# Kernel tuning notes

Measured on AMD Instinct MI355X. Metric: run time of the kernel, lower is better.

Reference implementation:

```python
import jax, jax.numpy as jnp
import numpy as np

N, E = 100000, 1600000
C_IN, C_HID, C_OUT = 64, 128, 64
EPS_MSG = 1e-7   # GENConv message eps
EPS_BN = 1e-5    # BatchNorm eps


def setup_inputs() -> dict:
    key = jax.random.key(0)
    ks = jax.random.split(key, 8)
    glorot = lambda k, shp, fan: jax.random.normal(k, shp, jnp.float32) * (1.0 / np.sqrt(fan))
    return dict(
        x=jax.random.normal(ks[0], (N, C_IN), jnp.float32),
        edge_index=jax.random.randint(ks[1], (2, E), 0, N, jnp.int32),
        edge_attr=jax.random.normal(ks[2], (E, C_IN), jnp.float32),
        pos=jax.random.normal(ks[3], (N, 3), jnp.float32),
        # GENConv internal MLP: Linear -> BN -> ReLU -> Linear
        W1=glorot(ks[4], (C_IN, C_HID), C_IN), b1=jnp.zeros((C_HID,), jnp.float32),
        g_mlp=jnp.ones((C_HID,), jnp.float32), be_mlp=jnp.zeros((C_HID,), jnp.float32),
        W2=glorot(ks[5], (C_HID, C_OUT), C_HID), b2=jnp.zeros((C_OUT,), jnp.float32),
        # block: BN -> SiLU -> Linear(no bias) -> BN -> SiLU
        g1=jnp.ones((C_OUT,), jnp.float32), be1=jnp.zeros((C_OUT,), jnp.float32),
        Wl=glorot(ks[6], (C_OUT, C_OUT), C_OUT),
        g2=jnp.ones((C_OUT,), jnp.float32), be2=jnp.zeros((C_OUT,), jnp.float32),
    )


def _bn(h, g, b):
    # training-mode batch norm over the node dimension
    m = h.mean(0)
    v = jnp.mean((h - m) ** 2, axis=0)
    return (h - m) * jax.lax.rsqrt(v + EPS_BN) * g + b


def reference(x, edge_index, edge_attr, pos, W1, b1, g_mlp, be_mlp, W2, b2,
              g1, be1, Wl, g2, be2):
    src, dst = edge_index[0], edge_index[1]
    # GENConv message: relu(x_j + e_attr) + eps, shape [E, C_IN]
    msg = jax.nn.relu(x[src] + edge_attr) + EPS_MSG
    # softmax aggregation over incoming edges per destination node (t = 1)
    mx = jax.ops.segment_max(msg, dst, num_segments=N)
    mx = jnp.where(jnp.isfinite(mx), mx, 0.0)  # guard empty segments
    ex = jnp.exp(msg - mx[dst])
    den = jax.ops.segment_sum(ex, dst, num_segments=N)
    w = ex / (den[dst] + 1e-16)
    aggr = jax.ops.segment_sum(msg * w, dst, num_segments=N)  # [N, C_IN]
    # root add + internal MLP (Linear -> BN -> ReLU -> Linear)
    h = aggr + x
    h = jax.nn.relu(_bn(h @ W1 + b1, g_mlp, be_mlp)) @ W2 + b2
    # block tail: BN -> SiLU -> Linear(no bias) -> BN -> SiLU
    h = jax.nn.silu(_bn(h, g1, be1))
    h = jax.nn.silu(_bn(h @ Wl, g2, be2))
    return h
```

## Files before the change

kernel.cpp:

```cpp
#include <hip/hip_runtime.h>

#define N_NODES 100000
#define E_EDGES 1600000
#define CIN 64
#define CHID 128
#define COUT 64
#define NT 64
#define NB ((N_NODES + NT - 1) / NT)
#define RBLK 64
#define CAP 128

__global__ void bucket_kernel(const int* __restrict__ ei, int* __restrict__ cnt,
                              int2* __restrict__ es) {
    int e = blockIdx.x * blockDim.x + threadIdx.x;
    if (e < E_EDGES) {
        int src = ei[e];
        int dst = ei[E_EDGES + e];
        int p = atomicAdd(&cnt[dst], 1);
        if (p < CAP) es[((long)dst << 7) + p] = make_int2(e, src);
    }
}

__global__ void gather_kernel(const float* __restrict__ x,
                              const float* __restrict__ ea,
                              const int2* __restrict__ es,
                              const int* __restrict__ cnt,
                              float* __restrict__ h0) {
    int node = (blockIdx.x * blockDim.x + threadIdx.x) >> 6;
    int lane = threadIdx.x & 63;
    if (node >= N_NODES) return;
    long s = (long)node << 7;
    int n = cnt[node];
    n = n > CAP ? CAP : n;
    float nm = 0.f, dn = 0.f;
    int p = 0;
    for (; p + 8 <= n; p += 8) {
        int2 q[8];
#pragma unroll
        for (int u = 0; u < 8; ++u) q[u] = es[s + p + u];
        float av[8], xv[8];
#pragma unroll
        for (int u = 0; u < 8; ++u) av[u] = ea[(long)q[u].x * CIN + lane];
#pragma unroll
        for (int u = 0; u < 8; ++u) xv[u] = x[(long)q[u].y * CIN + lane];
#pragma unroll
        for (int u = 0; u < 8; ++u) {
            float m = fmaxf(xv[u] + av[u], 0.f) + 1e-7f;
            float ex = __expf(m);
            nm = fmaf(m, ex, nm);
            dn += ex;
        }
    }
    for (; p + 4 <= n; p += 4) {
        int2 q[4];
#pragma unroll
        for (int u = 0; u < 4; ++u) q[u] = es[s + p + u];
        float av[4], xv[4];
#pragma unroll
        for (int u = 0; u < 4; ++u) av[u] = ea[(long)q[u].x * CIN + lane];
#pragma unroll
        for (int u = 0; u < 4; ++u) xv[u] = x[(long)q[u].y * CIN + lane];
#pragma unroll
        for (int u = 0; u < 4; ++u) {
            float m = fmaxf(xv[u] + av[u], 0.f) + 1e-7f;
            float ex = __expf(m);
            nm = fmaf(m, ex, nm);
            dn += ex;
        }
    }
    for (; p < n; ++p) {
        int2 q = es[s + p];
        float m = fmaxf(x[(long)q.y * CIN + lane] + ea[(long)q.x * CIN + lane], 0.f) + 1e-7f;
        float ex = __expf(m);
        nm = fmaf(m, ex, nm);
        dn += ex;
    }
    h0[(long)node * CIN + lane] = nm / (dn + 1e-16f) + x[(long)node * CIN + lane];
}

__global__ void reduce_slab_kernel(const float* __restrict__ P, int totrows,
                                   int rows_per, float* __restrict__ Q,
                                   float* __restrict__ mr, int C, float invN,
                                   int* __restrict__ ticket) {
    int C2 = blockDim.x;
    int t = threadIdx.x;
    long r0 = (long)blockIdx.x * rows_per;
    long r1 = r0 + rows_per;
    if (r1 > totrows) r1 = totrows;
    {
        float s0 = 0.f, s1 = 0.f, s2 = 0.f, s3 = 0.f;
        long r = r0;
        for (; r + 4 <= r1; r += 4) {
            s0 += P[(r + 0) * C2 + t];
            s1 += P[(r + 1) * C2 + t];
            s2 += P[(r + 2) * C2 + t];
            s3 += P[(r + 3) * C2 + t];
        }
        for (; r < r1; ++r) s0 += P[r * C2 + t];
        Q[(long)blockIdx.x * C2 + t] = (s0 + s1) + (s2 + s3);
    }
    __threadfence();
    __shared__ int lastFlag;
    if (t == 0) lastFlag = (atomicAdd(ticket, 1) == (int)gridDim.x - 1);
    __syncthreads();
    if (!lastFlag) return;
    __threadfence();
    float s0 = 0.f, s1 = 0.f, s2 = 0.f, s3 = 0.f;
    for (int r = 0; r < RBLK; r += 4) {
        s0 += Q[(long)(r + 0) * C2 + t];
        s1 += Q[(long)(r + 1) * C2 + t];
        s2 += Q[(long)(r + 2) * C2 + t];
        s3 += Q[(long)(r + 3) * C2 + t];
    }
    __shared__ float sm[256];
    sm[t] = (s0 + s1) + (s2 + s3);
    __syncthreads();
    if (t < C) {
        float m = sm[t] * invN;
        float v = sm[C + t] * invN - m * m;
        mr[t] = m;
        mr[C + t] = rsqrtf(fmaxf(v, 0.f) + 1e-5f);
    }
}

__global__ void __launch_bounds__(256) gemm1_kernel(
        const float* __restrict__ h0, const float* __restrict__ W1,
        const float* __restrict__ b1, float* __restrict__ t1,
        float* __restrict__ P) {
    __shared__ float sW[CIN * CHID];
    __shared__ float sh[NT * CIN];
    int tid = threadIdx.x;
    int nbase = blockIdx.x * NT;
    for (int i = tid * 4; i < CIN * CHID; i += 1024)
        *(float4*)&sW[i] = *(const float4*)&W1[i];
    for (int i = tid * 4; i < NT * CIN; i += 1024) {
        int node = nbase + (i >> 6);
        float4 v = make_float4(0.f, 0.f, 0.f, 0.f);
        if (node < N_NODES) v = *(const float4*)&h0[(long)node * CIN + (i & 63)];
        *(float4*)&sh[i] = v;
    }
    __syncthreads();
    int js = (tid & 31) * 4;
    int r  = tid >> 5;
    float4 bb = *(const float4*)&b1[js];
    float acc[8][4];
#pragma unroll
    for (int i = 0; i < 8; ++i) { acc[i][0]=bb.x; acc[i][1]=bb.y; acc[i][2]=bb.z; acc[i][3]=bb.w; }
#pragma unroll 4
    for (int k = 0; k < CIN; ++k) {
        float4 w = *(float4*)&sW[k * CHID + js];
#pragma unroll
        for (int i = 0; i < 8; ++i) {
            float a = sh[(r * 8 + i) * CIN + k];
            acc[i][0] = fmaf(a, w.x, acc[i][0]);
            acc[i][1] = fmaf(a, w.y, acc[i][1]);
            acc[i][2] = fmaf(a, w.z, acc[i][2]);
            acc[i][3] = fmaf(a, w.w, acc[i][3]);
        }
    }
    float s1[4] = {0,0,0,0}, s2[4] = {0,0,0,0};
#pragma unroll
    for (int i = 0; i < 8; ++i) {
        int node = nbase + r * 8 + i;
        if (node < N_NODES) {
            *(float4*)&t1[(long)node * CHID + js] =
                make_float4(acc[i][0], acc[i][1], acc[i][2], acc[i][3]);
#pragma unroll
            for (int jj = 0; jj < 4; ++jj) {
                s1[jj] += acc[i][jj];
                s2[jj] += acc[i][jj] * acc[i][jj];
            }
        }
    }
    __syncthreads();
    float* red = sW;
    *(float4*)&red[r * 128 + js]        = make_float4(s1[0], s1[1], s1[2], s1[3]);
    *(float4*)&red[1024 + r * 128 + js] = make_float4(s2[0], s2[1], s2[2], s2[3]);
    __syncthreads();
    {
        int base = (tid < 128) ? tid : (1024 + tid - 128);
        float v = 0.f;
#pragma unroll
        for (int rr = 0; rr < 8; ++rr) v += red[base + rr * 128];
        P[(long)blockIdx.x * 256 + tid] = v;
    }
}

__global__ void __launch_bounds__(256) gemm2_kernel(
        const float* __restrict__ t1, const float* __restrict__ mr1,
        const float* __restrict__ g, const float* __restrict__ be,
        const float* __restrict__ W2, const float* __restrict__ b2,
        float* __restrict__ h2, float* __restrict__ P) {
    __shared__ float sW[CHID * COUT];
    __shared__ float sr[NT * CHID];
    int tid = threadIdx.x;
    int nbase = blockIdx.x * NT;
    for (int i = tid * 4; i < CHID * COUT; i += 1024)
        *(float4*)&sW[i] = *(const float4*)&W2[i];
    for (int i = tid * 4; i < NT * CHID; i += 1024) {
        int node = nbase + (i >> 7);
        int j = i & 127;
        float4 v = make_float4(0.f, 0.f, 0.f, 0.f);
        if (node < N_NODES) {
            v = *(const float4*)&t1[(long)node * CHID + j];
            float4 mn = *(const float4*)&mr1[j];
            float4 rq = *(const float4*)&mr1[CHID + j];
            float4 gg = *(const float4*)&g[j];
            float4 bb = *(const float4*)&be[j];
            v.x = fmaxf((v.x - mn.x) * rq.x * gg.x + bb.x, 0.f);
            v.y = fmaxf((v.y - mn.y) * rq.y * gg.y + bb.y, 0.f);
            v.z = fmaxf((v.z - mn.z) * rq.z * gg.z + bb.z, 0.f);
            v.w = fmaxf((v.w - mn.w) * rq.w * gg.w + bb.w, 0.f);
        }
        *(float4*)&sr[i] = v;
    }
    __syncthreads();
    int js = (tid & 15) * 4;
    int r  = tid >> 4;
    float4 bb = *(const float4*)&b2[js];
    float acc[4][4];
#pragma unroll
    for (int i = 0; i < 4; ++i) { acc[i][0]=bb.x; acc[i][1]=bb.y; acc[i][2]=bb.z; acc[i][3]=bb.w; }
#pragma unroll 4
    for (int k = 0; k < CHID; ++k) {
        float4 w = *(float4*)&sW[k * COUT + js];
#pragma unroll
        for (int i = 0; i < 4; ++i) {
            float a = sr[(r * 4 + i) * CHID + k];
            acc[i][0] = fmaf(a, w.x, acc[i][0]);
            acc[i][1] = fmaf(a, w.y, acc[i][1]);
            acc[i][2] = fmaf(a, w.z, acc[i][2]);
            acc[i][3] = fmaf(a, w.w, acc[i][3]);
        }
    }
    float s1[4] = {0,0,0,0}, s2[4] = {0,0,0,0};
#pragma unroll
    for (int i = 0; i < 4; ++i) {
        int node = nbase + r * 4 + i;
        if (node < N_NODES) {
            *(float4*)&h2[(long)node * COUT + js] =
                make_float4(acc[i][0], acc[i][1], acc[i][2], acc[i][3]);
#pragma unroll
            for (int jj = 0; jj < 4; ++jj) {
                s1[jj] += acc[i][jj];
                s2[jj] += acc[i][jj] * acc[i][jj];
            }
        }
    }
    __syncthreads();
    float* red = sW;
    *(float4*)&red[r * 64 + js]        = make_float4(s1[0], s1[1], s1[2], s1[3]);
    *(float4*)&red[1024 + r * 64 + js] = make_float4(s2[0], s2[1], s2[2], s2[3]);
    __syncthreads();
    if (tid < 128) {
        int base = (tid < 64) ? tid : (1024 + tid - 64);
        float v = 0.f;
#pragma unroll
        for (int rr = 0; rr < 16; ++rr) v += red[base + rr * 64];
        P[(long)blockIdx.x * 128 + tid] = v;
    }
}

__global__ void __launch_bounds__(256) gemm3_kernel(
        const float* __restrict__ h2, const float* __restrict__ mr2,
        const float* __restrict__ g, const float* __restrict__ be,
        const float* __restrict__ Wl,
        float* __restrict__ t3, float* __restrict__ P) {
    __shared__ float sW[COUT * COUT];
    __shared__ float sr[NT * COUT];
    int tid = threadIdx.x;
    int nbase = blockIdx.x * NT;
    for (int i = tid * 4; i < COUT * COUT; i += 1024)
        *(float4*)&sW[i] = *(const float4*)&Wl[i];
    for (int i = tid * 4; i < NT * COUT; i += 1024) {
        int node = nbase + (i >> 6);
        int j = i & 63;
        float4 v = make_float4(0.f, 0.f, 0.f, 0.f);
        if (node < N_NODES) {
            v = *(const float4*)&h2[(long)node * COUT + j];
            float4 mn = *(const float4*)&mr2[j];
            float4 rq = *(const float4*)&mr2[COUT + j];
            float4 gg = *(const float4*)&g[j];
            float4 bb = *(const float4*)&be[j];
            v.x = (v.x - mn.x) * rq.x * gg.x + bb.x;
            v.y = (v.y - mn.y) * rq.y * gg.y + bb.y;
            v.z = (v.z - mn.z) * rq.z * gg.z + bb.z;
            v.w = (v.w - mn.w) * rq.w * gg.w + bb.w;
            v.x = v.x / (1.f + __expf(-v.x));
            v.y = v.y / (1.f + __expf(-v.y));
            v.z = v.z / (1.f + __expf(-v.z));
            v.w = v.w / (1.f + __expf(-v.w));
        }
        *(float4*)&sr[i] = v;
    }
    __syncthreads();
    int js = (tid & 15) * 4;
    int r  = tid >> 4;
    float acc[4][4];
#pragma unroll
    for (int i = 0; i < 4; ++i) { acc[i][0]=0.f; acc[i][1]=0.f; acc[i][2]=0.f; acc[i][3]=0.f; }
#pragma unroll 4
    for (int k = 0; k < COUT; ++k) {
        float4 w = *(float4*)&sW[k * COUT + js];
#pragma unroll
        for (int i = 0; i < 4; ++i) {
            float a = sr[(r * 4 + i) * COUT + k];
            acc[i][0] = fmaf(a, w.x, acc[i][0]);
            acc[i][1] = fmaf(a, w.y, acc[i][1]);
            acc[i][2] = fmaf(a, w.z, acc[i][2]);
            acc[i][3] = fmaf(a, w.w, acc[i][3]);
        }
    }
    float s1[4] = {0,0,0,0}, s2[4] = {0,0,0,0};
#pragma unroll
    for (int i = 0; i < 4; ++i) {
        int node = nbase + r * 4 + i;
        if (node < N_NODES) {
            *(float4*)&t3[(long)node * COUT + js] =
                make_float4(acc[i][0], acc[i][1], acc[i][2], acc[i][3]);
#pragma unroll
            for (int jj = 0; jj < 4; ++jj) {
                s1[jj] += acc[i][jj];
                s2[jj] += acc[i][jj] * acc[i][jj];
            }
        }
    }
    __syncthreads();
    float* red = sW;
    *(float4*)&red[r * 64 + js]        = make_float4(s1[0], s1[1], s1[2], s1[3]);
    *(float4*)&red[1024 + r * 64 + js] = make_float4(s2[0], s2[1], s2[2], s2[3]);
    __syncthreads();
    if (tid < 128) {
        int base = (tid < 64) ? tid : (1024 + tid - 64);
        float v = 0.f;
#pragma unroll
        for (int rr = 0; rr < 16; ++rr) v += red[base + rr * 64];
        P[(long)blockIdx.x * 128 + tid] = v;
    }
}

__global__ void final_kernel(const float* __restrict__ t3, const float* __restrict__ mr3,
                             const float* __restrict__ g, const float* __restrict__ be,
                             float* __restrict__ out) {
    long i = ((long)blockIdx.x * blockDim.x + threadIdx.x) * 4;
    int j = (int)(i & 63);
    float4 v = *(const float4*)&t3[i];
    float4 mn = *(const float4*)&mr3[j];
    float4 rq = *(const float4*)&mr3[COUT + j];
    float4 gg = *(const float4*)&g[j];
    float4 bb = *(const float4*)&be[j];
    v.x = (v.x - mn.x) * rq.x * gg.x + bb.x;
    v.y = (v.y - mn.y) * rq.y * gg.y + bb.y;
    v.z = (v.z - mn.z) * rq.z * gg.z + bb.z;
    v.w = (v.w - mn.w) * rq.w * gg.w + bb.w;
    v.x = v.x / (1.f + __expf(-v.x));
    v.y = v.y / (1.f + __expf(-v.y));
    v.z = v.z / (1.f + __expf(-v.z));
    v.w = v.w / (1.f + __expf(-v.w));
    *(float4*)&out[i] = v;
}

extern "C" void kernel_launch(void* const* d_in, const int* in_sizes, int n_in,
                              void* d_out, int out_size, void* d_ws, size_t ws_size,
                              hipStream_t stream) {
    const float* x   = (const float*)d_in[0];
    const int*   ei  = (const int*)d_in[1];
    const float* ea  = (const float*)d_in[2];
    const float* W1  = (const float*)d_in[4];
    const float* b1  = (const float*)d_in[5];
    const float* gm  = (const float*)d_in[6];
    const float* bm  = (const float*)d_in[7];
    const float* W2  = (const float*)d_in[8];
    const float* b2  = (const float*)d_in[9];
    const float* g1  = (const float*)d_in[10];
    const float* be1 = (const float*)d_in[11];
    const float* Wl  = (const float*)d_in[12];
    const float* g2  = (const float*)d_in[13];
    const float* be2 = (const float*)d_in[14];
    float* out = (float*)d_out;

    float* h0   = (float*)d_ws;
    float* t1   = h0 + (long)N_NODES * CIN;
    float* h2   = t1 + (long)N_NODES * CHID;
    float* t3   = h0;
    float* Sfin = h2 + (long)N_NODES * COUT;
    float* Q    = Sfin + 512;
    int*   cnt  = (int*)(Q + RBLK * 256);
    int*   tickets = cnt + N_NODES;
    long   es_off = ((long)(N_NODES * CIN) + (long)N_NODES * CHID + (long)N_NODES * COUT
                     + 512 + RBLK * 256 + N_NODES + 4 + 255) & ~255L;
    int2*  es   = (int2*)((float*)d_ws + es_off);
    float* P1 = h2;
    float* P2 = h0;
    float* P3 = t1;

    const float invN = 1.f / N_NODES;

    hipMemsetAsync(cnt, 0, ((size_t)N_NODES + 4) * sizeof(int), stream);

    bucket_kernel<<<(E_EDGES + 255) / 256, 256, 0, stream>>>(ei, cnt, es);
    gather_kernel<<<(N_NODES * 64 + 255) / 256, 256, 0, stream>>>(x, ea, es, cnt, h0);

    const int rpA = (NB + RBLK - 1) / RBLK;

    gemm1_kernel<<<NB, 256, 0, stream>>>(h0, W1, b1, t1, P1);
    reduce_slab_kernel<<<RBLK, 256, 0, stream>>>(P1, NB, rpA, Q, Sfin, CHID, invN, tickets + 0);
    gemm2_kernel<<<NB, 256, 0, stream>>>(t1, Sfin, gm, bm, W2, b2, h2, P2);
    reduce_slab_kernel<<<RBLK, 128, 0, stream>>>(P2, NB, rpA, Q, Sfin + 256, COUT, invN, tickets + 1);
    gemm3_kernel<<<NB, 256, 0, stream>>>(h2, Sfin + 256, g1, be1, Wl, t3, P3);
    reduce_slab_kernel<<<RBLK, 128, 0, stream>>>(P3, NB, rpA, Q, Sfin + 384, COUT, invN, tickets + 2);
    final_kernel<<<(N_NODES * COUT / 4) / 256, 256, 0, stream>>>(t3, Sfin + 384, g2, be2, out);
}
```

Baseline: 380.7 us.

## Vectorize edge gather with float4 lanes over 4 edge groups and vectorize bucketing

The gather kernel now assigns each wavefront lane four channels (float4) and splits the 64 lanes into four edge groups. This gives wider loads, 32 edges in flight per iteration, nontemporal loads for edge attributes, and a shuffle reduction across groups at the end. The bucket kernel handles four edges per thread using int4 loads of the edge index. The aim is to raise memory-level parallelism and cut load instruction count on the bandwidth-bound gather. The cost is predicated padding work for nodes with few edges and extra cross-lane shuffles.

```diff
diff --git a/kernel.cpp b/kernel.cpp
--- a/kernel.cpp
+++ b/kernel.cpp
@@ -10,15 +10,22 @@
 #define RBLK 64
 #define CAP 128
 
+typedef float f32x4 __attribute__((ext_vector_type(4)));
+
 __global__ void bucket_kernel(const int* __restrict__ ei, int* __restrict__ cnt,
                               int2* __restrict__ es) {
-    int e = blockIdx.x * blockDim.x + threadIdx.x;
-    if (e < E_EDGES) {
-        int src = ei[e];
-        int dst = ei[E_EDGES + e];
-        int p = atomicAdd(&cnt[dst], 1);
-        if (p < CAP) es[((long)dst << 7) + p] = make_int2(e, src);
-    }
+    int e4 = (blockIdx.x * blockDim.x + threadIdx.x) * 4;
+    if (e4 >= E_EDGES) return;
+    int4 s = *(const int4*)&ei[e4];
+    int4 d = *(const int4*)&ei[E_EDGES + e4];
+    int p0 = atomicAdd(&cnt[d.x], 1);
+    if (p0 < CAP) es[((long)d.x << 7) + p0] = make_int2(e4 + 0, s.x);
+    int p1 = atomicAdd(&cnt[d.y], 1);
+    if (p1 < CAP) es[((long)d.y << 7) + p1] = make_int2(e4 + 1, s.y);
+    int p2 = atomicAdd(&cnt[d.z], 1);
+    if (p2 < CAP) es[((long)d.z << 7) + p2] = make_int2(e4 + 2, s.z);
+    int p3 = atomicAdd(&cnt[d.w], 1);
+    if (p3 < CAP) es[((long)d.w << 7) + p3] = make_int2(e4 + 3, s.w);
 }
 
 __global__ void gather_kernel(const float* __restrict__ x,
@@ -29,53 +36,60 @@
     int node = (blockIdx.x * blockDim.x + threadIdx.x) >> 6;
     int lane = threadIdx.x & 63;
     if (node >= N_NODES) return;
+    int eg = lane >> 4;
+    int ch = (lane & 15) * 4;
     long s = (long)node << 7;
     int n = cnt[node];
     n = n > CAP ? CAP : n;
-    float nm = 0.f, dn = 0.f;
-    int p = 0;
-    for (; p + 8 <= n; p += 8) {
-        int2 q[8];
-#pragma unroll
-        for (int u = 0; u < 8; ++u) q[u] = es[s + p + u];
-        float av[8], xv[8];
-#pragma unroll
-        for (int u = 0; u < 8; ++u) av[u] = ea[(long)q[u].x * CIN + lane];
-#pragma unroll
-        for (int u = 0; u < 8; ++u) xv[u] = x[(long)q[u].y * CIN + lane];
+    f32x4 xr = *(const f32x4*)&x[(long)node * CIN + ch];
+    if (n == 0) {
+        if (eg == 0) *(f32x4*)&h0[(long)node * CIN + ch] = xr;
+        return;
+    }
+    f32x4 nm = (f32x4)(0.f);
+    f32x4 dn = (f32x4)(0.f);
+    for (int p = 0; p < n; p += 32) {
+        int2 q[8]; bool act[8];
 #pragma unroll
         for (int u = 0; u < 8; ++u) {
-            float m = fmaxf(xv[u] + av[u], 0.f) + 1e-7f;
-            float ex = __expf(m);
-            nm = fmaf(m, ex, nm);
-            dn += ex;
-        }
-    }
-    for (; p + 4 <= n; p += 4) {
-        int2 q[4];
-#pragma unroll
-        for (int u = 0; u < 4; ++u) q[u] = es[s + p + u];
-        float av[4], xv[4];
-#pragma unroll
-        for (int u = 0; u < 4; ++u) av[u] = ea[(long)q[u].x * CIN + lane];
-#pragma unroll
-        for (int u = 0; u < 4; ++u) xv[u] = x[(long)q[u].y * CIN + lane];
-#pragma unroll
-        for (int u = 0; u < 4; ++u) {
-            float m = fmaxf(xv[u] + av[u], 0.f) + 1e-7f;
-            float ex = __expf(m);
-            nm = fmaf(m, ex, nm);
-            dn += ex;
-        }
-    }
-    for (; p < n; ++p) {
-        int2 q = es[s + p];
-        float m = fmaxf(x[(long)q.y * CIN + lane] + ea[(long)q.x * CIN + lane], 0.f) + 1e-7f;
-        float ex = __expf(m);
-        nm = fmaf(m, ex, nm);
-        dn += ex;
-    }
-    h0[(long)node * CIN + lane] = nm / (dn + 1e-16f) + x[(long)node * CIN + lane];
+            int idx = p + u * 4 + eg;
+            act[u] = idx < n;
+            idx = act[u] ? idx : n - 1;
+            q[u] = es[s + idx];
+        }
+        f32x4 av[8], xv[8];
+#pragma unroll
+        for (int u = 0; u < 8; ++u)
+            av[u] = __builtin_nontemporal_load(
+                        reinterpret_cast<const f32x4*>(ea + (long)q[u].x * CIN + ch));
+#pragma unroll
+        for (int u = 0; u < 8; ++u)
+            xv[u] = *reinterpret_cast<const f32x4*>(x + (long)q[u].y * CIN + ch);
+#pragma unroll
+        for (int u = 0; u < 8; ++u) {
+#pragma unroll
+            for (int c = 0; c < 4; ++c) {
+                float m = fmaxf(xv[u][c] + av[u][c], 0.f) + 1e-7f;
+                float e = act[u] ? __expf(m) : 0.f;
+                nm[c] = fmaf(m, e, nm[c]);
+                dn[c] += e;
+            }
+        }
+    }
+#pragma unroll
+    for (int mask = 16; mask <= 32; mask <<= 1) {
+#pragma unroll
+        for (int c = 0; c < 4; ++c) {
+            nm[c] += __shfl_xor(nm[c], mask);
+            dn[c] += __shfl_xor(dn[c], mask);
+        }
+    }
+    if (eg == 0) {
+        f32x4 o;
+#pragma unroll
+        for (int c = 0; c < 4; ++c) o[c] = nm[c] / (dn[c] + 1e-16f) + xr[c];
+        *(f32x4*)&h0[(long)node * CIN + ch] = o;
+    }
 }
 
 __global__ void reduce_slab_kernel(const float* __restrict__ P, int totrows,
@@ -398,7 +412,7 @@
 
     hipMemsetAsync(cnt, 0, ((size_t)N_NODES + 4) * sizeof(int), stream);
 
-    bucket_kernel<<<(E_EDGES + 255) / 256, 256, 0, stream>>>(ei, cnt, es);
+    bucket_kernel<<<(E_EDGES / 4 + 255) / 256, 256, 0, stream>>>(ei, cnt, es);
     gather_kernel<<<(N_NODES * 64 + 255) / 256, 256, 0, stream>>>(x, ea, es, cnt, h0);
 
     const int rpA = (NB + RBLK - 1) / RBLK;
```

Result: slower. 391.3 us (+2.8%).
